# Performance work log

Measured on AMD Instinct MI355X. Metric: run time of the kernel, lower is better.

## Reference

```python
import jax, jax.numpy as jnp
import numpy as np

SEQ, D = 4096, 1024  # vector_size == dimension == 1024


def setup_inputs() -> dict:
    key = jax.random.key(0)
    ks = jax.random.split(key, 7)
    s = 1.0 / np.sqrt(D)
    return {
        "X": jax.random.normal(ks[0], (SEQ, D), dtype=jnp.float32),
        "Wq": jax.random.normal(ks[1], (D, D), dtype=jnp.float32) * s,
        "bq": jax.random.normal(ks[2], (D,), dtype=jnp.float32) * s,
        "Wk": jax.random.normal(ks[3], (D, D), dtype=jnp.float32) * s,
        "bk": jax.random.normal(ks[4], (D,), dtype=jnp.float32) * s,
        "Wv": jax.random.normal(ks[5], (D, D), dtype=jnp.float32) * s,
        "bv": jax.random.normal(ks[6], (D,), dtype=jnp.float32) * s,
    }


def reference(X, Wq, bq, Wk, bk, Wv, bv):
    # Batched QKV projections (nn.Linear: x @ W^T + b), replacing the per-vector loop.
    Q = X @ Wq.T + bq            # [S, D]
    K = X @ Wk.T + bk            # [S, D]
    V = X @ Wv.T + bv            # [S, D]
    scale = 1.0 / jnp.sqrt(jnp.asarray(D, dtype=X.dtype))
    scores = (Q @ K.T) * scale   # [S, S]
    attn = jax.nn.softmax(scores, axis=1)
    return attn @ V              # [S, D]
```

## Files before the change

kernel.cpp:

```cpp
#include <hip/hip_runtime.h>
#include <hip/hip_bf16.h>
#include <stdint.h>


typedef __bf16 bf16_t;
typedef __bf16 bf16x4 __attribute__((ext_vector_type(4)));
typedef __bf16 bf16x8 __attribute__((ext_vector_type(8)));
typedef float f32x4 __attribute__((ext_vector_type(4)));

#define AS1 __attribute__((address_space(1)))
#define AS3 __attribute__((address_space(3)))

__device__ __forceinline__ void async_ld16(const void* g, void* l) {
  __builtin_amdgcn_global_load_lds((AS1 void*)g, (AS3 void*)l, 16, 0, 0);
}

template <int MODE>
__device__ void gemm_core(bf16_t* As, bf16_t* Bs, const int t, const int m0,
                          const int n0, const int k0, const int zz,
                          const bf16_t* __restrict__ A,
                          const bf16_t* __restrict__ B, const int ld,
                          const int Klen, bf16_t* __restrict__ o0,
                          bf16_t* __restrict__ o1, bf16_t* __restrict__ o2,
                          const float* __restrict__ b0,
                          const float* __restrict__ b1,
                          const float* __restrict__ b2,
                          float* __restrict__ fout,
                          float* __restrict__ rowsum) {
  constexpr int BN = 128, BK = 64;
  constexpr int NF = BN / 32;
  constexpr int KS = BK / 32;
  constexpr int CH = BK / 8;
  constexpr int RS = 256 / CH;

  const int lane = t & 63;
  const int wave = t >> 6;
  const int wm = wave >> 1;
  const int wn = wave & 1;
  const int q = lane >> 4;
  const int l16 = lane & 15;
  const int wnoff = wn * (BN / 2);

  const f32x4 zero4 = {0.f, 0.f, 0.f, 0.f};
  f32x4 acc[4][NF];
#pragma unroll
  for (int i = 0; i < 4; ++i)
#pragma unroll
    for (int j = 0; j < NF; ++j) acc[i][j] = zero4;

  const int srow = t / CH;
  const int schunk = (t % CH) ^ (srow & 7);
  const bf16_t* Ab = A + (size_t)(m0 + srow) * ld + k0 + schunk * 8;
  const bf16_t* Bb = B + (size_t)(n0 + srow) * ld + k0 + schunk * 8;
  bf16_t* Asl = As + t * 8;
  bf16_t* Bsl = Bs + t * 8;

  const int xf = l16 & 7;
  const int ar = wm * 64 + l16;
  const int br = wnoff + l16;

  for (int kt = 0; kt < Klen; kt += BK) {
#pragma unroll
    for (int rr = 0; rr < 128 / RS; ++rr)
      async_ld16(Ab + kt + (size_t)(rr * RS) * ld, Asl + rr * RS * BK);
#pragma unroll
    for (int rr = 0; rr < BN / RS; ++rr)
      async_ld16(Bb + kt + (size_t)(rr * RS) * ld, Bsl + rr * RS * BK);
    __syncthreads();

#pragma unroll
    for (int s = 0; s < KS; ++s) {
      bf16x8 fa[4], fb[NF];
#pragma unroll
      for (int im = 0; im < 4; ++im)
        fa[im] = *(const bf16x8*)(As + (ar + im * 16) * BK +
                                  (((s * 4 + q) ^ xf) * 8));
#pragma unroll
      for (int j = 0; j < NF; ++j)
        fb[j] = *(const bf16x8*)(Bs + (br + j * 16) * BK +
                                 (((s * 4 + q) ^ xf) * 8));
#pragma unroll
      for (int im = 0; im < 4; ++im)
#pragma unroll
        for (int j = 0; j < NF; ++j)
          acc[im][j] = __builtin_amdgcn_mfma_f32_16x16x32_bf16(
              fa[im], fb[j], acc[im][j], 0, 0, 0);
    }
    __syncthreads();
  }

  const int mBase = m0 + wm * 64 + q * 4;

  if constexpr (MODE == 0) {
    const int sel = n0 >> 10;
    const int nl0 = (n0 & 1023) + wnoff + l16;
    if (sel < 2) {
      const float* bias = (sel == 0) ? b0 : b1;
      const float sc = (sel == 0) ? 0.03125f : 1.0f;
      bf16_t* dst = (sel == 0) ? o0 : o1;
#pragma unroll
      for (int j = 0; j < NF; ++j) {
        const int nl = nl0 + j * 16;
        const float bb = bias[nl];
#pragma unroll
        for (int im = 0; im < 4; ++im) {
          const int mr = mBase + im * 16;
#pragma unroll
          for (int r = 0; r < 4; ++r)
            dst[(size_t)(mr + r) * 1024 + nl] =
                (bf16_t)((acc[im][j][r] + bb) * sc);
        }
      }
    } else {
      bf16_t* vs = As;
      const int dg0 = (n0 & 1023);
#pragma unroll
      for (int h = 0; h < 2; ++h) {
        if (wn == h) {
#pragma unroll
          for (int j = 0; j < NF; ++j) {
            const int dl = j * 16 + l16;
            const float bb = b2[dg0 + h * 64 + dl];
#pragma unroll
            for (int im = 0; im < 4; ++im) {
              bf16x4 v;
#pragma unroll
              for (int r = 0; r < 4; ++r) v[r] = (bf16_t)(acc[im][j][r] + bb);
              *(bf16x4*)(vs + dl * 136 + wm * 64 + im * 16 + q * 4) = v;
            }
          }
        }
        __syncthreads();
#pragma unroll
        for (int rr = 0; rr < 4; ++rr) {
          const int task = rr * 256 + t;
          const int row = task >> 4, ck = task & 15;
          *(bf16x8*)(o2 + (size_t)(dg0 + h * 64 + row) * 4096 + m0 + ck * 8) =
              *(const bf16x8*)(vs + row * 136 + ck * 8);
        }
        __syncthreads();
      }
    }
  } else if constexpr (MODE == 1) {
    float ps[4][4];
#pragma unroll
    for (int im = 0; im < 4; ++im)
#pragma unroll
      for (int r = 0; r < 4; ++r) ps[im][r] = 0.f;
#pragma unroll
    for (int j = 0; j < NF; ++j) {
      const int n = n0 + wnoff + j * 16 + l16;
#pragma unroll
      for (int im = 0; im < 4; ++im) {
        const int mr = mBase + im * 16;
#pragma unroll
        for (int r = 0; r < 4; ++r) {
          const float e = __expf(acc[im][j][r]);
          ps[im][r] += e;
          o0[(size_t)(mr + r) * 4096 + n] = (bf16_t)e;
        }
      }
    }
#pragma unroll
    for (int im = 0; im < 4; ++im)
#pragma unroll
      for (int r = 0; r < 4; ++r) {
        float v = ps[im][r];
        v += __shfl_xor(v, 1);
        v += __shfl_xor(v, 2);
        v += __shfl_xor(v, 4);
        v += __shfl_xor(v, 8);
        ps[im][r] = v;
      }
    if (l16 == 0) {
#pragma unroll
      for (int im = 0; im < 4; ++im)
#pragma unroll
        for (int r = 0; r < 4; ++r)
          atomicAdd(rowsum + mBase + im * 16 + r, ps[im][r]);
    }
  } else {
    float inv[4][4];
#pragma unroll
    for (int im = 0; im < 4; ++im)
#pragma unroll
      for (int r = 0; r < 4; ++r)
        inv[im][r] = 1.0f / rowsum[mBase + im * 16 + r];
    if (zz < 3) {
      bf16_t* pp = (zz == 0) ? o0 : ((zz == 1) ? o1 : o2);
#pragma unroll
      for (int im = 0; im < 4; ++im) {
        const int mr = mBase + im * 16;
#pragma unroll
        for (int j = 0; j < NF; ++j) {
          const int n = n0 + wnoff + j * 16 + l16;
#pragma unroll
          for (int r = 0; r < 4; ++r)
            pp[(size_t)(mr + r) * 1024 + n] =
                (bf16_t)(acc[im][j][r] * inv[im][r]);
        }
      }
    } else {
#pragma unroll
      for (int im = 0; im < 4; ++im) {
        const int mr = mBase + im * 16;
#pragma unroll
        for (int j = 0; j < NF; ++j) {
          const int n = n0 + wnoff + j * 16 + l16;
#pragma unroll
          for (int r = 0; r < 4; ++r)
            fout[(size_t)(mr + r) * 1024 + n] = acc[im][j][r] * inv[im][r];
        }
      }
    }
  }
}

template <int MODE>
__global__ __launch_bounds__(256, 2) void gemm_sep(
    const bf16_t* __restrict__ A, const bf16_t* __restrict__ B, const int ld,
    const int Klen,
    bf16_t* __restrict__ o0, bf16_t* __restrict__ o1, bf16_t* __restrict__ o2,
    const float* __restrict__ b0, const float* __restrict__ b1,
    const float* __restrict__ b2, float* __restrict__ fout,
    float* __restrict__ rowsum) {
  __shared__ bf16_t smem[2 * 128 * 64];
  bf16_t* As = smem;
  bf16_t* Bs = smem + 128 * 64;
  int m0, n0, k0 = 0, zz = 0;
  if constexpr (MODE == 1) {
    const int bid = blockIdx.y * 32 + blockIdx.x;
    const int xcd = bid & 7, sl = bid >> 3;
    m0 = ((xcd >> 2) * 16 + (sl >> 3)) * 128;
    n0 = ((xcd & 3) * 8 + (sl & 7)) * 128;
  } else if constexpr (MODE == 2) {
    const int lin = blockIdx.x;
    const int xcd = lin & 7, s = lin >> 3;
    zz = xcd >> 1;
    m0 = ((xcd & 1) * 16 + (s >> 3)) * 128;
    n0 = (s & 7) * 128;
    k0 = zz * Klen;
  } else {
    n0 = blockIdx.x * 128;
    m0 = blockIdx.y * 128;
  }
  gemm_core<MODE>(As, Bs, threadIdx.x, m0, n0, k0, zz, A, B, ld, Klen, o0, o1,
                  o2, b0, b1, b2, fout, rowsum);
}

__global__ __launch_bounds__(256) void cvt_all(
    const float* __restrict__ X, const float* __restrict__ Wq,
    const float* __restrict__ Wk, const float* __restrict__ Wv,
    bf16_t* __restrict__ Xb, bf16_t* __restrict__ Wb,
    float* __restrict__ rowsum) {
  int i = blockIdx.x * 256 + threadIdx.x;
  if (i >= 1835008) {
    rowsum[i - 1835008] = 0.f;
    return;
  }
  const float* src;
  bf16_t* dst;
  int off;
  if (i < 1048576) {
    src = X; dst = Xb; off = i;
  } else {
    const int w = i - 1048576;
    const int sel = w >> 18;
    off = w & 0x3FFFF;
    src = (sel == 0) ? Wq : ((sel == 1) ? Wk : Wv);
    dst = Wb + (size_t)sel * (1024 * 1024);
  }
  const float4 v = ((const float4*)src)[off];
  bf16x4 o;
  o[0] = (bf16_t)v.x; o[1] = (bf16_t)v.y; o[2] = (bf16_t)v.z; o[3] = (bf16_t)v.w;
  ((bf16x4*)dst)[off] = o;
}

__global__ __launch_bounds__(256) void reduce_out(
    const bf16_t* __restrict__ p0, const bf16_t* __restrict__ p1,
    const bf16_t* __restrict__ p2, float* __restrict__ out) {
  const int i = blockIdx.x * 256 + threadIdx.x;
  const bf16x8 a = ((const bf16x8*)p0)[i];
  const bf16x8 b = ((const bf16x8*)p1)[i];
  const bf16x8 c = ((const bf16x8*)p2)[i];
  float4 lo = ((const float4*)out)[2 * i];
  float4 hi = ((const float4*)out)[2 * i + 1];
  lo.x += (float)a[0] + (float)b[0] + (float)c[0];
  lo.y += (float)a[1] + (float)b[1] + (float)c[1];
  lo.z += (float)a[2] + (float)b[2] + (float)c[2];
  lo.w += (float)a[3] + (float)b[3] + (float)c[3];
  hi.x += (float)a[4] + (float)b[4] + (float)c[4];
  hi.y += (float)a[5] + (float)b[5] + (float)c[5];
  hi.z += (float)a[6] + (float)b[6] + (float)c[6];
  hi.w += (float)a[7] + (float)b[7] + (float)c[7];
  ((float4*)out)[2 * i] = lo;
  ((float4*)out)[2 * i + 1] = hi;
}

extern "C" void kernel_launch(void* const* d_in, const int* in_sizes, int n_in,
                              void* d_out, int out_size, void* d_ws,
                              size_t ws_size, hipStream_t stream) {
  const int S = 4096, D = 1024;
  const float* X  = (const float*)d_in[0];
  const float* Wq = (const float*)d_in[1];
  const float* bq = (const float*)d_in[2];
  const float* Wk = (const float*)d_in[3];
  const float* bk = (const float*)d_in[4];
  const float* Wv = (const float*)d_in[5];
  const float* bv = (const float*)d_in[6];
  float* out = (float*)d_out;

  bf16_t* Xb = (bf16_t*)d_ws;
  bf16_t* Wb = Xb + (size_t)S * D;
  bf16_t* Qb = Wb + (size_t)3 * D * D;
  bf16_t* Kb = Qb + (size_t)S * D;
  bf16_t* Vt = Kb + (size_t)S * D;
  bf16_t* Sc = Vt + (size_t)D * S;
  float* rowsum = (float*)(Sc + (size_t)S * S);

  cvt_all<<<7184, 256, 0, stream>>>(X, Wq, Wk, Wv, Xb, Wb, rowsum);

  gemm_sep<0><<<dim3(24, 32), 256, 0, stream>>>(
      Xb, Wb, D, D, Qb, Kb, Vt, bq, bk, bv, nullptr, nullptr);
  gemm_sep<1><<<dim3(32, 32), 256, 0, stream>>>(
      Qb, Kb, D, D, Sc, nullptr, nullptr, nullptr, nullptr, nullptr, nullptr,
      rowsum);
  gemm_sep<2><<<1024, 256, 0, stream>>>(
      Sc, Vt, S, S / 4, Xb, Qb, Kb, nullptr, nullptr, nullptr, out, rowsum);
  reduce_out<<<S * D / 8 / 256, 256, 0, stream>>>(Xb, Qb, Kb, out);
}
```

Measured before the change: 208.9 us.

## Replace GEMM kernels with 256x256-tile 8-wave double-buffered pipelined MFMA kernel

Replaces the 128x128 single-buffered GEMM with a 256x256-tile, 512-thread kernel. It double-buffers 128KB of dynamic LDS and interleaves async global-to-LDS loads for the tile two steps ahead with four MFMA phases, using explicit barriers, waitcnt and setprio. Larger tiles raise data reuse per block and the pipeline is meant to hide load latency behind compute. The cost is fewer blocks (192-256, near the CU count), heavy register use for 32 accumulators per lane, and fragile manual vmcnt accounting.

After: 218.2 us. +4.4%, slower.

```diff
diff --git a/kernel.cpp b/kernel.cpp
--- a/kernel.cpp
+++ b/kernel.cpp
@@ -15,96 +15,208 @@
   __builtin_amdgcn_global_load_lds((AS1 void*)g, (AS3 void*)l, 16, 0, 0);
 }
 
+#define SBAR() __builtin_amdgcn_sched_barrier(0)
+#define BARRIER()                 \
+  do {                            \
+    SBAR();                       \
+    __builtin_amdgcn_s_barrier(); \
+    SBAR();                       \
+  } while (0)
+#define LGKM0()                                         \
+  do {                                                  \
+    asm volatile("s_waitcnt lgkmcnt(0)" ::: "memory");  \
+    SBAR();                                             \
+  } while (0)
+
 template <int MODE>
-__device__ void gemm_core(bf16_t* As, bf16_t* Bs, const int t, const int m0,
-                          const int n0, const int k0, const int zz,
-                          const bf16_t* __restrict__ A,
-                          const bf16_t* __restrict__ B, const int ld,
-                          const int Klen, bf16_t* __restrict__ o0,
-                          bf16_t* __restrict__ o1, bf16_t* __restrict__ o2,
-                          const float* __restrict__ b0,
-                          const float* __restrict__ b1,
-                          const float* __restrict__ b2,
-                          float* __restrict__ fout,
-                          float* __restrict__ rowsum) {
-  constexpr int BN = 128, BK = 64;
-  constexpr int NF = BN / 32;
-  constexpr int KS = BK / 32;
-  constexpr int CH = BK / 8;
-  constexpr int RS = 256 / CH;
-
+__global__ __launch_bounds__(512, 2) void gemm8(
+    const bf16_t* __restrict__ A, const bf16_t* __restrict__ B, const int ld,
+    const int Klen, bf16_t* __restrict__ o0, bf16_t* __restrict__ o1,
+    bf16_t* __restrict__ o2, const float* __restrict__ b0,
+    const float* __restrict__ b1, const float* __restrict__ b2,
+    float* __restrict__ fout, float* __restrict__ rowsum) {
+  extern __shared__ bf16_t smem[];
+
+  const int t = threadIdx.x;
   const int lane = t & 63;
   const int wave = t >> 6;
-  const int wm = wave >> 1;
-  const int wn = wave & 1;
+  const int wm = wave >> 2;
+  const int wn = wave & 3;
   const int q = lane >> 4;
   const int l16 = lane & 15;
-  const int wnoff = wn * (BN / 2);
-
+  const int xf = l16 & 7;
+
+  int m0, n0, k0 = 0, zz = 0;
+  const int bid = blockIdx.x;
+  if constexpr (MODE == 0) {
+    const int x = bid & 7, sl = bid >> 3;
+    m0 = ((x >> 1) * 4 + (sl & 3)) * 256;
+    n0 = ((x & 1) * 6 + (sl >> 2)) * 256;
+  } else if constexpr (MODE == 1) {
+    const int x = bid & 7, sl = bid >> 3;
+    m0 = ((x >> 2) * 8 + (sl >> 2)) * 256;
+    n0 = ((x & 3) * 4 + (sl & 3)) * 256;
+  } else {
+    const int x = bid & 7, sl = bid >> 3;
+    zz = x >> 1;
+    m0 = ((x & 1) * 8 + (sl >> 2)) * 256;
+    n0 = (sl & 3) * 256;
+    k0 = zz * Klen;
+  }
+
+  const int srow = t >> 3;
+  const int c8s = ((t & 7) ^ (srow & 7)) * 8;
+  const bf16_t* Ab = A + (size_t)(m0 + srow) * ld + k0 + c8s;
+  const bf16_t* Bb = B + (size_t)(n0 + srow) * ld + k0 + c8s;
+  const int tl8 = t * 8;
+
+  const int aoff = (wm * 128 + l16) * 64;
+  const int boff = (wn * 64 + l16) * 64;
+  const int c0 = (q ^ xf) * 8;
+  const int c1 = ((4 + q) ^ xf) * 8;
+
+  f32x4 acc[8][4];
   const f32x4 zero4 = {0.f, 0.f, 0.f, 0.f};
-  f32x4 acc[4][NF];
-#pragma unroll
-  for (int i = 0; i < 4; ++i)
-#pragma unroll
-    for (int j = 0; j < NF; ++j) acc[i][j] = zero4;
-
-  const int srow = t / CH;
-  const int schunk = (t % CH) ^ (srow & 7);
-  const bf16_t* Ab = A + (size_t)(m0 + srow) * ld + k0 + schunk * 8;
-  const bf16_t* Bb = B + (size_t)(n0 + srow) * ld + k0 + schunk * 8;
-  bf16_t* Asl = As + t * 8;
-  bf16_t* Bsl = Bs + t * 8;
-
-  const int xf = l16 & 7;
-  const int ar = wm * 64 + l16;
-  const int br = wnoff + l16;
-
-  for (int kt = 0; kt < Klen; kt += BK) {
-#pragma unroll
-    for (int rr = 0; rr < 128 / RS; ++rr)
-      async_ld16(Ab + kt + (size_t)(rr * RS) * ld, Asl + rr * RS * BK);
-#pragma unroll
-    for (int rr = 0; rr < BN / RS; ++rr)
-      async_ld16(Bb + kt + (size_t)(rr * RS) * ld, Bsl + rr * RS * BK);
-    __syncthreads();
-
-#pragma unroll
-    for (int s = 0; s < KS; ++s) {
-      bf16x8 fa[4], fb[NF];
-#pragma unroll
-      for (int im = 0; im < 4; ++im)
-        fa[im] = *(const bf16x8*)(As + (ar + im * 16) * BK +
-                                  (((s * 4 + q) ^ xf) * 8));
-#pragma unroll
-      for (int j = 0; j < NF; ++j)
-        fb[j] = *(const bf16x8*)(Bs + (br + j * 16) * BK +
-                                 (((s * 4 + q) ^ xf) * 8));
-#pragma unroll
-      for (int im = 0; im < 4; ++im)
-#pragma unroll
-        for (int j = 0; j < NF; ++j)
-          acc[im][j] = __builtin_amdgcn_mfma_f32_16x16x32_bf16(
-              fa[im], fb[j], acc[im][j], 0, 0, 0);
-    }
-    __syncthreads();
-  }
-
-  const int mBase = m0 + wm * 64 + q * 4;
+#pragma unroll
+  for (int i = 0; i < 8; ++i)
+#pragma unroll
+    for (int j = 0; j < 4; ++j) acc[i][j] = zero4;
+
+  const int NT = Klen >> 6;
+  bf16_t* buf0 = smem;
+  bf16_t* buf1 = smem + 32768;
+
+  async_ld16(Ab, buf0 + tl8);
+  async_ld16(Ab + (size_t)128 * ld, buf0 + 128 * 64 + tl8);
+  async_ld16(Bb, buf0 + 16384 + tl8);
+  async_ld16(Bb + (size_t)64 * ld, buf0 + 16384 + 64 * 64 + tl8);
+  async_ld16(Bb + (size_t)128 * ld, buf0 + 16384 + 128 * 64 + tl8);
+  async_ld16(Bb + (size_t)192 * ld, buf0 + 16384 + 192 * 64 + tl8);
+  async_ld16(Ab + (size_t)64 * ld, buf0 + 64 * 64 + tl8);
+  async_ld16(Ab + (size_t)192 * ld, buf0 + 192 * 64 + tl8);
+  async_ld16(Ab + 64, buf1 + tl8);
+  async_ld16(Ab + (size_t)128 * ld + 64, buf1 + 128 * 64 + tl8);
+  async_ld16(Bb + 64, buf1 + 16384 + tl8);
+  async_ld16(Bb + (size_t)64 * ld + 64, buf1 + 16384 + 64 * 64 + tl8);
+  async_ld16(Bb + (size_t)128 * ld + 64, buf1 + 16384 + 128 * 64 + tl8);
+  async_ld16(Bb + (size_t)192 * ld + 64, buf1 + 16384 + 192 * 64 + tl8);
+  asm volatile("s_waitcnt vmcnt(6)" ::: "memory");
+  BARRIER();
+
+  for (int T = 0; T < NT; ++T) {
+    bf16_t* Ac = (T & 1) ? buf1 : buf0;
+    bf16_t* An = (T & 1) ? buf0 : buf1;
+    bf16_t* Bc = Ac + 16384;
+    const int k1 = (T + 1) << 6;
+    const int k2 = (T + 2) << 6;
+    const bool s1 = (T + 1) < NT;
+    const bool s2 = (T + 2) < NT;
+
+    bf16x8 raA[4][2], raB[4][2], rb[4][2];
+
+#pragma unroll
+    for (int im = 0; im < 4; ++im) {
+      raA[im][0] = *(const bf16x8*)(Ac + aoff + im * 1024 + c0);
+      raA[im][1] = *(const bf16x8*)(Ac + aoff + im * 1024 + c1);
+    }
+#pragma unroll
+    for (int j = 0; j < 4; ++j)
+      rb[j][0] = *(const bf16x8*)(Bc + boff + j * 1024 + c0);
+    if (s1) {
+      async_ld16(Ab + (size_t)64 * ld + k1, An + 64 * 64 + tl8);
+      async_ld16(Ab + (size_t)192 * ld + k1, An + 192 * 64 + tl8);
+    }
+    BARRIER();
+    LGKM0();
+    __builtin_amdgcn_s_setprio(1);
+#pragma unroll
+    for (int im = 0; im < 4; ++im)
+#pragma unroll
+      for (int j = 0; j < 4; ++j)
+        acc[im][j] = __builtin_amdgcn_mfma_f32_16x16x32_bf16(
+            raA[im][0], rb[j][0], acc[im][j], 0, 0, 0);
+    __builtin_amdgcn_s_setprio(0);
+    BARRIER();
+
+#pragma unroll
+    for (int im = 0; im < 4; ++im)
+      raB[im][0] = *(const bf16x8*)(Ac + aoff + (im + 4) * 1024 + c0);
+#pragma unroll
+    for (int j = 0; j < 4; ++j)
+      rb[j][1] = *(const bf16x8*)(Bc + boff + j * 1024 + c1);
+    if (s2) {
+      async_ld16(Ab + k2, Ac + tl8);
+      async_ld16(Ab + (size_t)128 * ld + k2, Ac + 128 * 64 + tl8);
+    }
+    BARRIER();
+    LGKM0();
+    __builtin_amdgcn_s_setprio(1);
+#pragma unroll
+    for (int im = 0; im < 4; ++im)
+#pragma unroll
+      for (int j = 0; j < 4; ++j)
+        acc[4 + im][j] = __builtin_amdgcn_mfma_f32_16x16x32_bf16(
+            raB[im][0], rb[j][0], acc[4 + im][j], 0, 0, 0);
+    __builtin_amdgcn_s_setprio(0);
+    BARRIER();
+
+#pragma unroll
+    for (int im = 0; im < 4; ++im)
+      raB[im][1] = *(const bf16x8*)(Ac + aoff + (im + 4) * 1024 + c1);
+    if (s2) {
+      async_ld16(Bb + k2, Bc + tl8);
+      async_ld16(Bb + (size_t)64 * ld + k2, Bc + 64 * 64 + tl8);
+    }
+    BARRIER();
+    LGKM0();
+    __builtin_amdgcn_s_setprio(1);
+#pragma unroll
+    for (int im = 0; im < 4; ++im)
+#pragma unroll
+      for (int j = 0; j < 4; ++j)
+        acc[im][j] = __builtin_amdgcn_mfma_f32_16x16x32_bf16(
+            raA[im][1], rb[j][1], acc[im][j], 0, 0, 0);
+    __builtin_amdgcn_s_setprio(0);
+    BARRIER();
+
+    if (s2) {
+      async_ld16(Bb + (size_t)128 * ld + k2, Bc + 128 * 64 + tl8);
+      async_ld16(Bb + (size_t)192 * ld + k2, Bc + 192 * 64 + tl8);
+    }
+    BARRIER();
+    LGKM0();
+    __builtin_amdgcn_s_setprio(1);
+#pragma unroll
+    for (int im = 0; im < 4; ++im)
+#pragma unroll
+      for (int j = 0; j < 4; ++j)
+        acc[4 + im][j] = __builtin_amdgcn_mfma_f32_16x16x32_bf16(
+            raB[im][1], rb[j][1], acc[4 + im][j], 0, 0, 0);
+    __builtin_amdgcn_s_setprio(0);
+    if (s2) {
+      asm volatile("s_waitcnt vmcnt(6)" ::: "memory");
+    } else {
+      asm volatile("s_waitcnt vmcnt(0)" ::: "memory");
+    }
+    BARRIER();
+  }
+
+  const int mW = m0 + wm * 128 + q * 4;
 
   if constexpr (MODE == 0) {
     const int sel = n0 >> 10;
-    const int nl0 = (n0 & 1023) + wnoff + l16;
+    const int nl0 = (n0 & 1023) + wn * 64 + l16;
     if (sel < 2) {
       const float* bias = (sel == 0) ? b0 : b1;
       const float sc = (sel == 0) ? 0.03125f : 1.0f;
       bf16_t* dst = (sel == 0) ? o0 : o1;
 #pragma unroll
-      for (int j = 0; j < NF; ++j) {
+      for (int j = 0; j < 4; ++j) {
         const int nl = nl0 + j * 16;
         const float bb = bias[nl];
 #pragma unroll
-        for (int im = 0; im < 4; ++im) {
-          const int mr = mBase + im * 16;
+        for (int im = 0; im < 8; ++im) {
+          const int mr = mW + im * 16;
 #pragma unroll
           for (int r = 0; r < 4; ++r)
             dst[(size_t)(mr + r) * 1024 + nl] =
@@ -112,47 +224,47 @@
         }
       }
     } else {
-      bf16_t* vs = As;
-      const int dg0 = (n0 & 1023);
+      bf16_t* vs = smem;
+      const int dg0 = n0 & 1023;
 #pragma unroll
       for (int h = 0; h < 2; ++h) {
-        if (wn == h) {
-#pragma unroll
-          for (int j = 0; j < NF; ++j) {
-            const int dl = j * 16 + l16;
-            const float bb = b2[dg0 + h * 64 + dl];
-#pragma unroll
-            for (int im = 0; im < 4; ++im) {
+        if ((wn >> 1) == h) {
+#pragma unroll
+          for (int j = 0; j < 4; ++j) {
+            const int dl = (wn & 1) * 64 + j * 16 + l16;
+            const float bb = b2[dg0 + h * 128 + dl];
+#pragma unroll
+            for (int im = 0; im < 8; ++im) {
               bf16x4 v;
 #pragma unroll
               for (int r = 0; r < 4; ++r) v[r] = (bf16_t)(acc[im][j][r] + bb);
-              *(bf16x4*)(vs + dl * 136 + wm * 64 + im * 16 + q * 4) = v;
+              *(bf16x4*)(vs + dl * 264 + wm * 128 + im * 16 + q * 4) = v;
             }
           }
         }
         __syncthreads();
 #pragma unroll
-        for (int rr = 0; rr < 4; ++rr) {
-          const int task = rr * 256 + t;
-          const int row = task >> 4, ck = task & 15;
-          *(bf16x8*)(o2 + (size_t)(dg0 + h * 64 + row) * 4096 + m0 + ck * 8) =
-              *(const bf16x8*)(vs + row * 136 + ck * 8);
+        for (int rr = 0; rr < 8; ++rr) {
+          const int task = rr * 512 + t;
+          const int row = task >> 5, ck = task & 31;
+          *(bf16x8*)(o2 + (size_t)(dg0 + h * 128 + row) * 4096 + m0 + ck * 8) =
+              *(const bf16x8*)(vs + row * 264 + ck * 8);
         }
         __syncthreads();
       }
     }
   } else if constexpr (MODE == 1) {
-    float ps[4][4];
-#pragma unroll
-    for (int im = 0; im < 4; ++im)
+    float ps[8][4];
+#pragma unroll
+    for (int im = 0; im < 8; ++im)
 #pragma unroll
       for (int r = 0; r < 4; ++r) ps[im][r] = 0.f;
 #pragma unroll
-    for (int j = 0; j < NF; ++j) {
-      const int n = n0 + wnoff + j * 16 + l16;
-#pragma unroll
-      for (int im = 0; im < 4; ++im) {
-        const int mr = mBase + im * 16;
+    for (int j = 0; j < 4; ++j) {
+      const int n = n0 + wn * 64 + j * 16 + l16;
+#pragma unroll
+      for (int im = 0; im < 8; ++im) {
+        const int mr = mW + im * 16;
 #pragma unroll
         for (int r = 0; r < 4; ++r) {
           const float e = __expf(acc[im][j][r]);
@@ -162,7 +274,7 @@
       }
     }
 #pragma unroll
-    for (int im = 0; im < 4; ++im)
+    for (int im = 0; im < 8; ++im)
 #pragma unroll
       for (int r = 0; r < 4; ++r) {
         float v = ps[im][r];
@@ -174,26 +286,26 @@
       }
     if (l16 == 0) {
 #pragma unroll
-      for (int im = 0; im < 4; ++im)
+      for (int im = 0; im < 8; ++im)
 #pragma unroll
         for (int r = 0; r < 4; ++r)
-          atomicAdd(rowsum + mBase + im * 16 + r, ps[im][r]);
+          atomicAdd(rowsum + mW + im * 16 + r, ps[im][r]);
     }
   } else {
-    float inv[4][4];
-#pragma unroll
-    for (int im = 0; im < 4; ++im)
+    float inv[8][4];
+#pragma unroll
+    for (int im = 0; im < 8; ++im)
 #pragma unroll
       for (int r = 0; r < 4; ++r)
-        inv[im][r] = 1.0f / rowsum[mBase + im * 16 + r];
+        inv[im][r] = 1.0f / rowsum[mW + im * 16 + r];
     if (zz < 3) {
       bf16_t* pp = (zz == 0) ? o0 : ((zz == 1) ? o1 : o2);
 #pragma unroll
-      for (int im = 0; im < 4; ++im) {
-        const int mr = mBase + im * 16;
-#pragma unroll
-        for (int j = 0; j < NF; ++j) {
-          const int n = n0 + wnoff + j * 16 + l16;
+      for (int im = 0; im < 8; ++im) {
+        const int mr = mW + im * 16;
+#pragma unroll
+        for (int j = 0; j < 4; ++j) {
+          const int n = n0 + wn * 64 + j * 16 + l16;
 #pragma unroll
           for (int r = 0; r < 4; ++r)
             pp[(size_t)(mr + r) * 1024 + n] =
@@ -202,11 +314,11 @@
       }
     } else {
 #pragma unroll
-      for (int im = 0; im < 4; ++im) {
-        const int mr = mBase + im * 16;
-#pragma unroll
-        for (int j = 0; j < NF; ++j) {
-          const int n = n0 + wnoff + j * 16 + l16;
+      for (int im = 0; im < 8; ++im) {
+        const int mr = mW + im * 16;
+#pragma unroll
+        for (int j = 0; j < 4; ++j) {
+          const int n = n0 + wn * 64 + j * 16 + l16;
 #pragma unroll
           for (int r = 0; r < 4; ++r)
             fout[(size_t)(mr + r) * 1024 + n] = acc[im][j][r] * inv[im][r];
@@ -214,38 +326,6 @@
       }
     }
   }
-}
-
-template <int MODE>
-__global__ __launch_bounds__(256, 2) void gemm_sep(
-    const bf16_t* __restrict__ A, const bf16_t* __restrict__ B, const int ld,
-    const int Klen,
-    bf16_t* __restrict__ o0, bf16_t* __restrict__ o1, bf16_t* __restrict__ o2,
-    const float* __restrict__ b0, const float* __restrict__ b1,
-    const float* __restrict__ b2, float* __restrict__ fout,
-    float* __restrict__ rowsum) {
-  __shared__ bf16_t smem[2 * 128 * 64];
-  bf16_t* As = smem;
-  bf16_t* Bs = smem + 128 * 64;
-  int m0, n0, k0 = 0, zz = 0;
-  if constexpr (MODE == 1) {
-    const int bid = blockIdx.y * 32 + blockIdx.x;
-    const int xcd = bid & 7, sl = bid >> 3;
-    m0 = ((xcd >> 2) * 16 + (sl >> 3)) * 128;
-    n0 = ((xcd & 3) * 8 + (sl & 7)) * 128;
-  } else if constexpr (MODE == 2) {
-    const int lin = blockIdx.x;
-    const int xcd = lin & 7, s = lin >> 3;
-    zz = xcd >> 1;
-    m0 = ((xcd & 1) * 16 + (s >> 3)) * 128;
-    n0 = (s & 7) * 128;
-    k0 = zz * Klen;
-  } else {
-    n0 = blockIdx.x * 128;
-    m0 = blockIdx.y * 128;
-  }
-  gemm_core<MODE>(As, Bs, threadIdx.x, m0, n0, k0, zz, A, B, ld, Klen, o0, o1,
-                  o2, b0, b1, b2, fout, rowsum);
 }
 
 __global__ __launch_bounds__(256) void cvt_all(
@@ -318,14 +398,28 @@
   bf16_t* Sc = Vt + (size_t)D * S;
   float* rowsum = (float*)(Sc + (size_t)S * S);
 
+  static int attr_set = 0;
+  if (!attr_set) {
+    attr_set = 1;
+    (void)hipFuncSetAttribute(reinterpret_cast<const void*>(gemm8<0>),
+                              hipFuncAttributeMaxDynamicSharedMemorySize,
+                              131072);
+    (void)hipFuncSetAttribute(reinterpret_cast<const void*>(gemm8<1>),
+                              hipFuncAttributeMaxDynamicSharedMemorySize,
+                              131072);
+    (void)hipFuncSetAttribute(reinterpret_cast<const void*>(gemm8<2>),
+                              hipFuncAttributeMaxDynamicSharedMemorySize,
+                              131072);
+  }
+
   cvt_all<<<7184, 256, 0, stream>>>(X, Wq, Wk, Wv, Xb, Wb, rowsum);
 
-  gemm_sep<0><<<dim3(24, 32), 256, 0, stream>>>(
+  gemm8<0><<<192, 512, 131072, stream>>>(
       Xb, Wb, D, D, Qb, Kb, Vt, bq, bk, bv, nullptr, nullptr);
-  gemm_sep<1><<<dim3(32, 32), 256, 0, stream>>>(
+  gemm8<1><<<256, 512, 131072, stream>>>(
       Qb, Kb, D, D, Sc, nullptr, nullptr, nullptr, nullptr, nullptr, nullptr,
       rowsum);
-  gemm_sep<2><<<1024, 256, 0, stream>>>(
+  gemm8<2><<<256, 512, 131072, stream>>>(
       Sc, Vt, S, S / 4, Xb, Qb, Kb, nullptr, nullptr, nullptr, out, rowsum);
   reduce_out<<<S * D / 8 / 256, 256, 0, stream>>>(Xb, Qb, Kb, out);
 }
```
